# Optimization experiments

Measured on AMD Instinct MI355X. Metric: run time of the kernel, lower is better.

## Reference

```python
import jax, jax.numpy as jnp
import numpy as np

V, T, C, H, L = 32000, 1024, 768, 12, 6
HS = C // H
B = 4
EPS = 1e-5


def layernorm(x, g, b):
    mu = jnp.mean(x, axis=-1, keepdims=True)
    var = jnp.mean(jnp.square(x - mu), axis=-1, keepdims=True)
    return (x - mu) * jax.lax.rsqrt(var + EPS) * g + b


def setup_inputs() -> dict:
    key = jax.random.key(0)
    ks = iter(jax.random.split(key, 24))
    s = lambda *sh: jax.random.normal(next(ks), sh, dtype=jnp.float32) * 0.02
    inp = {
        "tokens": jax.random.randint(next(ks), (B, T), 0, V, dtype=jnp.int64),
        "tok_emb": s(V, C),
        "pos_emb": s(T, C),
        "ln1_g": jnp.ones((L, C), jnp.float32), "ln1_b": jnp.zeros((L, C), jnp.float32),
        "wq": s(L, C, C), "wk": s(L, C, C), "wv": s(L, C, C),
        "wo": s(L, C, C), "bo": jnp.zeros((L, C), jnp.float32),
        "ln2_g": jnp.ones((L, C), jnp.float32), "ln2_b": jnp.zeros((L, C), jnp.float32),
        "w1": s(L, C, 4 * C), "b1": jnp.zeros((L, 4 * C), jnp.float32),
        "w2": s(L, 4 * C, C), "b2": jnp.zeros((L, C), jnp.float32),
        "lnf_g": jnp.ones((C,), jnp.float32), "lnf_b": jnp.zeros((C,), jnp.float32),
        "lm_w": s(C, V), "lm_b": jnp.zeros((V,), jnp.float32),
    }
    return inp


def reference(tokens, tok_emb, pos_emb, ln1_g, ln1_b, wq, wk, wv, wo, bo,
              ln2_g, ln2_b, w1, b1, w2, b2, lnf_g, lnf_b, lm_w, lm_b):
    x = tok_emb[tokens] + pos_emb[:T]  # [B,T,C]
    causal = jnp.tril(jnp.ones((T, T), bool))
    scale = HS ** -0.5
    for l in range(L):
        h = layernorm(x, ln1_g[l], ln1_b[l])
        q = (h @ wq[l]).reshape(B, T, H, HS)
        k = (h @ wk[l]).reshape(B, T, H, HS)
        v = (h @ wv[l]).reshape(B, T, H, HS)
        att = jnp.einsum("bthd,bshd->bhts", q, k) * scale
        att = jnp.where(causal, att, -jnp.inf)
        wei = jax.nn.softmax(att, axis=-1)
        o = jnp.einsum("bhts,bshd->bthd", wei, v).reshape(B, T, C)
        x = o @ wo[l] + bo[l] + x
        h2 = layernorm(x, ln2_g[l], ln2_b[l])
        x = jax.nn.relu(h2 @ w1[l] + b1[l]) @ w2[l] + b2[l] + x
    x = layernorm(x, lnf_g, lnf_b)
    logits = x @ lm_w + lm_b  # [B,T,V]
    return logits
```

## Files before the change

### kernel.cpp

```cpp
#include <hip/hip_runtime.h>

static constexpr int kV = 32000, kT = 1024, kC = 768, kH = 12, kL = 6, kB = 4;
static constexpr int kF = 3072;
static constexpr int kM = kB * kT;
static constexpr float kNEG = -30000.f;

typedef __attribute__((ext_vector_type(8))) __bf16 bf16x8;
typedef __attribute__((ext_vector_type(4))) float  f32x4;

#define DEV __device__ __forceinline__

DEV void gload16(const void* g, void* l) {
  __builtin_amdgcn_global_load_lds((__attribute__((address_space(1))) void*)(g),
                                   (__attribute__((address_space(3))) void*)(l), 16, 0, 0);
}

__global__ __launch_bounds__(192) void embed_k(const int* __restrict__ tokens,
                                               const float* __restrict__ tok_emb,
                                               const float* __restrict__ pos_emb,
                                               float* __restrict__ x) {
  int row = blockIdx.x, tid = threadIdx.x;
  int tok = tokens[row];
  int t   = row & (kT - 1);
  const float4* te = (const float4*)(tok_emb + (size_t)tok * kC);
  const float4* pe = (const float4*)(pos_emb + (size_t)t * kC);
  float4 a = te[tid], p = pe[tid];
  float4 r; r.x = a.x + p.x; r.y = a.y + p.y; r.z = a.z + p.z; r.w = a.w + p.w;
  ((float4*)(x + (size_t)row * kC))[tid] = r;
}

__global__ __launch_bounds__(192) void ln_k(const float* __restrict__ x,
                                            const float* __restrict__ g,
                                            const float* __restrict__ b,
                                            __bf16* __restrict__ out) {
  int row = blockIdx.x, tid = threadIdx.x;
  float4 v = ((const float4*)(x + (size_t)row * kC))[tid];
  float s = v.x + v.y + v.z + v.w;
#pragma unroll
  for (int m = 1; m < 64; m <<= 1) s += __shfl_xor(s, m, 64);
  __shared__ float red1[3], red2[3];
  int wid = tid >> 6;
  if ((tid & 63) == 0) red1[wid] = s;
  __syncthreads();
  float mu = (red1[0] + red1[1] + red1[2]) * (1.f / kC);
  float d0 = v.x - mu, d1 = v.y - mu, d2 = v.z - mu, d3 = v.w - mu;
  float q = d0 * d0 + d1 * d1 + d2 * d2 + d3 * d3;
#pragma unroll
  for (int m = 1; m < 64; m <<= 1) q += __shfl_xor(q, m, 64);
  if ((tid & 63) == 0) red2[wid] = q;
  __syncthreads();
  float var = (red2[0] + red2[1] + red2[2]) * (1.f / kC);
  float rs = rsqrtf(var + 1e-5f);
  float4 gv = ((const float4*)g)[tid];
  float4 bv = ((const float4*)b)[tid];
  float o0 = d0 * rs * gv.x + bv.x;
  float o1 = d1 * rs * gv.y + bv.y;
  float o2 = d2 * rs * gv.z + bv.z;
  float o3 = d3 * rs * gv.w + bv.w;
  ushort4 pk;
  unsigned short* pp = (unsigned short*)&pk;
  __bf16 t0 = (__bf16)o0; pp[0] = *(unsigned short*)&t0;
  __bf16 t1 = (__bf16)o1; pp[1] = *(unsigned short*)&t1;
  __bf16 t2 = (__bf16)o2; pp[2] = *(unsigned short*)&t2;
  __bf16 t3 = (__bf16)o3; pp[3] = *(unsigned short*)&t3;
  ((ushort4*)(out + (size_t)row * kC))[tid] = pk;
}

__global__ __launch_bounds__(256) void convT_k(const float* __restrict__ in,
                                               __bf16* __restrict__ out,
                                               int R, int Cc, size_t in_ls, size_t out_ls) {
  __shared__ float tile[32][33];
  const float* inp  = in  + (size_t)blockIdx.z * in_ls;
  __bf16*      outp = out + (size_t)blockIdx.z * out_ls;
  int r0 = blockIdx.y * 32, c0 = blockIdx.x * 32;
  int tx = threadIdx.x & 31, ty = threadIdx.x >> 5;
#pragma unroll
  for (int i = 0; i < 32; i += 8)
    tile[ty + i][tx] = inp[(size_t)(r0 + ty + i) * Cc + c0 + tx];
  __syncthreads();
  int wx = threadIdx.x & 15, wy = threadIdx.x >> 4;
#pragma unroll
  for (int i = 0; i < 32; i += 16) {
    int oc = wy + i;
    __bf16 a = (__bf16)tile[wx * 2][oc];
    __bf16 c = (__bf16)tile[wx * 2 + 1][oc];
    ushort2 pk;
    unsigned short* pp = (unsigned short*)&pk;
    pp[0] = *(unsigned short*)&a;
    pp[1] = *(unsigned short*)&c;
    *(ushort2*)(&outp[(size_t)(c0 + oc) * R + r0 + wx * 2]) = pk;
  }
}

DEV void tile_decode(int gx, int gy, int& mt, int& nt) {
  int nwg  = gx * gy;
  int wgid = blockIdx.y * gx + blockIdx.x;
  int q8 = nwg >> 3;
  int xcd = wgid & 7, loc = wgid >> 3;
  int sid = xcd * q8 + loc;
  int band = gx << 3;
  int c = sid / band, rem = sid % band;
  nt = rem >> 3;
  mt = (c << 3) + (rem & 7);
}

__global__ __launch_bounds__(512, 1) void gemmHD_k(const __bf16* __restrict__ A,
                                                   const __bf16* __restrict__ Bt,
                                                   const float* __restrict__ bias,
                                                   float* __restrict__ Cout,
                                                   int M, int N, int K) {
  __shared__ char lds[131072];
  int tid = threadIdx.x, lane = tid & 63, wid = tid >> 6;
  int wm = wid >> 2, wn = wid & 3;
  int mt, ntile;
  tile_decode(gridDim.x, gridDim.y, mt, ntile);
  int m0 = mt * 256, n0 = ntile * 256;
  int fr = lane & 15, fg = lane >> 4;
  f32x4 acc[8][4] = {};
  const size_t ldab = (size_t)K * 2;
  int nt = K >> 6;

  auto STAGE = [&](char* base, int t) {
    int k0 = t << 6;
#pragma unroll
    for (int it = 0; it < 4; ++it) {
      int oo  = tid * 16 + it * 8192;
      int row = oo >> 7;
      int cb  = (oo & 127) ^ ((row & 7) << 4);
      gload16((const char*)A + (size_t)(m0 + row) * ldab + (size_t)k0 * 2 + cb,
              base + it * 8192 + wid * 1024);
    }
#pragma unroll
    for (int it = 0; it < 4; ++it) {
      int oo  = tid * 16 + it * 8192;
      int row = oo >> 7;
      int cb  = (oo & 127) ^ ((row & 7) << 4);
      gload16((const char*)Bt + (size_t)(n0 + row) * ldab + (size_t)k0 * 2 + cb,
              base + 32768 + it * 8192 + wid * 1024);
    }
  };

  STAGE(lds, 0);
  asm volatile("s_waitcnt vmcnt(0)" ::: "memory");
  __builtin_amdgcn_sched_barrier(0);
  __builtin_amdgcn_s_barrier();

  for (int t = 0; t < nt; ++t) {
    char* base = lds + (t & 1) * 65536;
    const char* Ab = base;
    const char* Bb = base + 32768;
    if (t + 1 < nt) STAGE(lds + ((t + 1) & 1) * 65536, t + 1);

    __builtin_amdgcn_s_setprio(1);
    bf16x8 bfr[4];
#pragma unroll
    for (int p = 0; p < 4; ++p) {
      const int ks = p >> 1, mh = p & 1;
      const int cc = ks * 64 + fg * 16;
      if (mh == 0) {
#pragma unroll
        for (int n = 0; n < 4; ++n) {
          int row = wn * 64 + n * 16 + fr;
          bfr[n] = *(const bf16x8*)(Bb + row * 128 + (cc ^ ((row & 7) << 4)));
        }
      }
      bf16x8 af[4];
#pragma unroll
      for (int i = 0; i < 4; ++i) {
        int row = wm * 128 + mh * 64 + i * 16 + fr;
        af[i] = *(const bf16x8*)(Ab + row * 128 + (cc ^ ((row & 7) << 4)));
      }
#pragma unroll
      for (int i = 0; i < 4; ++i)
#pragma unroll
        for (int n = 0; n < 4; ++n)
          acc[mh * 4 + i][n] = __builtin_amdgcn_mfma_f32_16x16x32_bf16(
              af[i], bfr[n], acc[mh * 4 + i][n], 0, 0, 0);
    }
    __builtin_amdgcn_s_setprio(0);

    __builtin_amdgcn_s_barrier();
    if (t + 1 < nt)
      asm volatile("s_waitcnt vmcnt(0)" ::: "memory");
    __builtin_amdgcn_sched_barrier(0);
    __builtin_amdgcn_s_barrier();
  }

#pragma unroll
  for (int mi = 0; mi < 8; ++mi) {
#pragma unroll
    for (int n = 0; n < 4; ++n) {
      int cg  = n0 + wn * 64 + n * 16 + fr;
      int rgb = m0 + wm * 128 + mi * 16 + fg * 4;
      float bv = bias[cg];
#pragma unroll
      for (int r = 0; r < 4; ++r)
        Cout[(size_t)(rgb + r) * N + cg] = acc[mi][n][r] + bv;
    }
  }
}

template <int EPI>
__global__ __launch_bounds__(256) void gemm128_k(const __bf16* __restrict__ A,
                                                 const __bf16* __restrict__ Bt,
                                                 const float* __restrict__ bias,
                                                 const float* res,
                                                 void* Cout,
                                                 int M, int N, int K) {
  __shared__ char lds[65536];
  int tid = threadIdx.x, lane = tid & 63, wid = tid >> 6;
  int wr = wid >> 1, wc = wid & 1;
  int mt, ntile;
  tile_decode(gridDim.x, gridDim.y, mt, ntile);
  int m0 = mt * 128, n0 = ntile * 128;
  int fr = lane & 15, fg = lane >> 4;
  f32x4 acc[4][4] = {};
  const size_t ldab = (size_t)K * 2;

  auto STAGE = [&](int buf, int t) {
    int k0 = t << 6;
    char* base = lds + buf * 32768;
#pragma unroll
    for (int it = 0; it < 4; ++it) {
      int oo  = tid * 16 + it * 4096;
      int row = oo >> 7;
      int cb  = (oo & 127) ^ ((row & 7) << 4);
      gload16((const char*)A  + (size_t)(m0 + row) * ldab + (size_t)k0 * 2 + cb,
              base + it * 4096 + wid * 1024);
      gload16((const char*)Bt + (size_t)(n0 + row) * ldab + (size_t)k0 * 2 + cb,
              base + 16384 + it * 4096 + wid * 1024);
    }
  };
  auto COMPUTE = [&](int buf) {
    char* base = lds + buf * 32768;
#pragma unroll
    for (int kk = 0; kk < 2; ++kk) {
      int cb = (kk * 64 + (fg << 4)) ^ ((lane & 7) << 4);
      bf16x8 af[4], bfr[4];
#pragma unroll
      for (int i = 0; i < 4; ++i) {
        af[i]  = *(const bf16x8*)(base         + (wr * 64 + i * 16 + fr) * 128 + cb);
        bfr[i] = *(const bf16x8*)(base + 16384 + (wc * 64 + i * 16 + fr) * 128 + cb);
      }
#pragma unroll
      for (int i = 0; i < 4; ++i)
#pragma unroll
        for (int j = 0; j < 4; ++j)
          acc[i][j] = __builtin_amdgcn_mfma_f32_16x16x32_bf16(af[i], bfr[j], acc[i][j], 0, 0, 0);
    }
  };

  int nt = K >> 6;
  STAGE(0, 0);
  STAGE(1, 1);
  asm volatile("s_waitcnt vmcnt(8)" ::: "memory");
  __builtin_amdgcn_sched_barrier(0);
  __builtin_amdgcn_s_barrier();
  int cur = 0;
  for (int t = 0; t < nt; ++t) {
    __builtin_amdgcn_s_setprio(1);
    COMPUTE(cur);
    __builtin_amdgcn_s_setprio(0);
    if (t + 1 < nt) {
      __builtin_amdgcn_s_barrier();
      if (t + 2 < nt) {
        STAGE(cur, t + 2);
        asm volatile("s_waitcnt vmcnt(8)" ::: "memory");
      } else {
        asm volatile("s_waitcnt vmcnt(0)" ::: "memory");
      }
      __builtin_amdgcn_sched_barrier(0);
      __builtin_amdgcn_s_barrier();
      cur ^= 1;
    }
  }

#pragma unroll
  for (int i = 0; i < 4; ++i) {
#pragma unroll
    for (int j = 0; j < 4; ++j) {
      int cg  = n0 + wc * 64 + j * 16 + fr;
      int rgb = m0 + wr * 64 + i * 16 + fg * 4;
      if constexpr (EPI == 4) {
        if (n0 < 1536) {
#pragma unroll
          for (int r = 0; r < 4; ++r)
            ((__bf16*)Cout)[(size_t)(rgb + r) * 1536 + cg] = (__bf16)acc[i][j][r];
        } else {
          int d = cg - 1536;
          ushort4 pk;
          unsigned short* pp = (unsigned short*)&pk;
#pragma unroll
          for (int r = 0; r < 4; ++r) {
            __bf16 bv = (__bf16)acc[i][j][r];
            pp[r] = *(unsigned short*)&bv;
          }
          __bf16* vT = (__bf16*)const_cast<float*>(res);
          *(ushort4*)(vT + (size_t)d * kM + rgb) = pk;
        }
      } else if constexpr (EPI == 1) {
        float bv = bias[cg];
#pragma unroll
        for (int r = 0; r < 4; ++r) {
          float v = acc[i][j][r] + bv;
          ((__bf16*)Cout)[(size_t)(rgb + r) * N + cg] = (__bf16)fmaxf(v, 0.f);
        }
      } else {
        float bv = bias[cg];
#pragma unroll
        for (int r = 0; r < 4; ++r) {
          float v = acc[i][j][r] + bv;
          size_t idx = (size_t)(rgb + r) * N + cg;
          ((float*)Cout)[idx] = v + res[idx];
        }
      }
    }
  }
}

__global__ __launch_bounds__(256) void attn_k(const __bf16* __restrict__ qk,
                                              const __bf16* __restrict__ vT,
                                              __bf16* __restrict__ optr) {
  __shared__ char lds[40960];
  int tid = threadIdx.x, lane = tid & 63, wid = tid >> 6;
  int hh = blockIdx.y, bb = blockIdx.z;
  int zy = bb * 12 + hh;
  int qt = (blockIdx.x + (zy >> 4) * 5 + (zy & 15)) & 15;
  size_t rowbase = (size_t)bb * kT;
  int qr = qt * 64 + wid * 16;
  char* Psw = lds + 32768 + wid * 2048;

  bf16x8 qf[2];
  {
    const __bf16* p = qk + (rowbase + qr + (lane & 15)) * (2 * kC) + hh * 64 + ((lane >> 4) * 8);
    qf[0] = *(const bf16x8*)p;
    qf[1] = *(const bf16x8*)(p + 32);
  }
  f32x4 oacc[4] = {};
  float mrun[4] = {kNEG, kNEG, kNEG, kNEG};
  float lrun[4] = {0.f, 0.f, 0.f, 0.f};

  bf16x8 kr[2], vr[2];
  auto LOADT = [&](int st) {
    int s0 = st * 64;
#pragma unroll
    for (int it = 0; it < 2; ++it) {
      int oo  = tid * 16 + it * 4096;
      int row = oo >> 7;
      int cb  = (oo & 127) ^ ((row & 7) << 4);
      kr[it] = *(const bf16x8*)((const char*)qk +
                 ((rowbase + s0 + row) * (2 * kC) + kC + hh * 64) * 2 + cb);
      vr[it] = *(const bf16x8*)((const char*)vT +
                 ((size_t)(hh * 64 + row) * kM + rowbase + s0) * 2 + cb);
    }
  };
  auto WRITET = [&](int buf) {
    char* b = lds + buf * 16384;
#pragma unroll
    for (int it = 0; it < 2; ++it) {
      int oo = tid * 16 + it * 4096;
      *(bf16x8*)(b + oo)        = kr[it];
      *(bf16x8*)(b + 8192 + oo) = vr[it];
    }
  };

  LOADT(0);
  WRITET(0);
  if (qt >= 1) LOADT(1);

  for (int st = 0; st <= qt; ++st) {
    int cur = st & 1;
    char* kb = lds + cur * 16384;
    char* vb = kb + 8192;
    __syncthreads();
    if (st + 1 <= qt) {
      WRITET(cur ^ 1);
      if (st + 2 <= qt) LOADT(st + 2);
    }

    int s0 = st * 64;
    f32x4 sacc[4] = {};
#pragma unroll
    for (int kk = 0; kk < 2; ++kk) {
      int cb = (kk * 64 + ((lane >> 4) << 4)) ^ ((lane & 7) << 4);
#pragma unroll
      for (int j = 0; j < 4; ++j) {
        bf16x8 kf = *(const bf16x8*)(kb + (j * 16 + (lane & 15)) * 128 + cb);
        sacc[j] = __builtin_amdgcn_mfma_f32_16x16x32_bf16(qf[kk], kf, sacc[j], 0, 0, 0);
      }
    }

    float pv[4][4], vm[4] = {kNEG, kNEG, kNEG, kNEG};
#pragma unroll
    for (int j = 0; j < 4; ++j) {
      int scol = s0 + j * 16 + (lane & 15);
#pragma unroll
      for (int r = 0; r < 4; ++r) {
        int qrow = qr + (lane >> 4) * 4 + r;
        float sv = sacc[j][r] * 0.125f;
        if (scol > qrow) sv = kNEG;
        pv[j][r] = sv;
        vm[r] = fmaxf(vm[r], sv);
      }
    }
#pragma unroll
    for (int r = 0; r < 4; ++r) {
      float v = vm[r];
      v = fmaxf(v, __shfl_xor(v, 1, 64)); v = fmaxf(v, __shfl_xor(v, 2, 64));
      v = fmaxf(v, __shfl_xor(v, 4, 64)); v = fmaxf(v, __shfl_xor(v, 8, 64));
      float mnew = fmaxf(mrun[r], v);
      float sc = __expf(mrun[r] - mnew);
      mrun[r] = mnew;
      lrun[r] *= sc;
      oacc[0][r] *= sc; oacc[1][r] *= sc; oacc[2][r] *= sc; oacc[3][r] *= sc;
      float rsum = 0.f;
#pragma unroll
      for (int j = 0; j < 4; ++j) {
        float p = __expf(pv[j][r] - mnew);
        pv[j][r] = p;
        rsum += p;
      }
      rsum += __shfl_xor(rsum, 1, 64); rsum += __shfl_xor(rsum, 2, 64);
      rsum += __shfl_xor(rsum, 4, 64); rsum += __shfl_xor(rsum, 8, 64);
      lrun[r] += rsum;
    }

#pragma unroll
    for (int j = 0; j < 4; ++j)
#pragma unroll
      for (int r = 0; r < 4; ++r) {
        int rloc = (lane >> 4) * 4 + r;
        int cbyt = (2 * (j * 16 + (lane & 15))) ^ ((rloc & 7) << 4);
        *(__bf16*)(Psw + rloc * 128 + cbyt) = (__bf16)pv[j][r];
      }

#pragma unroll
    for (int kk = 0; kk < 2; ++kk) {
      int cb = (kk * 64 + ((lane >> 4) << 4)) ^ ((lane & 7) << 4);
      bf16x8 pf = *(const bf16x8*)(Psw + (lane & 15) * 128 + cb);
#pragma unroll
      for (int j = 0; j < 4; ++j) {
        bf16x8 vf = *(const bf16x8*)(vb + (j * 16 + (lane & 15)) * 128 + cb);
        oacc[j] = __builtin_amdgcn_mfma_f32_16x16x32_bf16(pf, vf, oacc[j], 0, 0, 0);
      }
    }
  }

#pragma unroll
  for (int r = 0; r < 4; ++r) {
    float inv = lrun[r] > 0.f ? 1.f / lrun[r] : 0.f;
#pragma unroll
    for (int j = 0; j < 4; ++j) {
      int cg = hh * 64 + j * 16 + (lane & 15);
      int rg = qr + (lane >> 4) * 4 + r;
      optr[(rowbase + rg) * kC + cg] = (__bf16)(oacc[j][r] * inv);
    }
  }
}

extern "C" void kernel_launch(void* const* d_in, const int* in_sizes, int n_in,
                              void* d_out, int out_size, void* d_ws, size_t ws_size,
                              hipStream_t stream) {
  (void)in_sizes; (void)n_in; (void)out_size; (void)ws_size;
  const int*   tokens  = (const int*)  d_in[0];
  const float* tok_emb = (const float*)d_in[1];
  const float* pos_emb = (const float*)d_in[2];
  const float* ln1_g   = (const float*)d_in[3];
  const float* ln1_b   = (const float*)d_in[4];
  const float* wq      = (const float*)d_in[5];
  const float* wk      = (const float*)d_in[6];
  const float* wv      = (const float*)d_in[7];
  const float* wo      = (const float*)d_in[8];
  const float* bo      = (const float*)d_in[9];
  const float* ln2_g   = (const float*)d_in[10];
  const float* ln2_b   = (const float*)d_in[11];
  const float* w1      = (const float*)d_in[12];
  const float* b1      = (const float*)d_in[13];
  const float* w2      = (const float*)d_in[14];
  const float* b2      = (const float*)d_in[15];
  const float* lnf_g   = (const float*)d_in[16];
  const float* lnf_b   = (const float*)d_in[17];
  const float* lm_w    = (const float*)d_in[18];
  const float* lm_b    = (const float*)d_in[19];
  float* out = (float*)d_out;

  char* ws = (char*)d_ws;
  size_t off = 0;
  auto alloc = [&](size_t bytes) -> char* {
    char* p = ws + off; off += (bytes + 255) & ~(size_t)255; return p;
  };
  float*  x    = (float*) alloc((size_t)kM * kC * 4);
  __bf16* h    = (__bf16*)alloc((size_t)kM * kC * 2);
  __bf16* qkvT = (__bf16*)alloc((size_t)kL * 3 * kC * kC * 2);
  __bf16* woT  = (__bf16*)alloc((size_t)kL * kC * kC * 2);
  __bf16* w1T  = (__bf16*)alloc((size_t)kL * kC * kF * 2);
  __bf16* w2T  = (__bf16*)alloc((size_t)kL * kC * kF * 2);
  __bf16* qkb  = (__bf16*)alloc((size_t)kM * 2 * kC * 2);
  __bf16* vTb  = (__bf16*)alloc((size_t)kC * kM * 2);
  __bf16* ob   = (__bf16*)alloc((size_t)kM * kC * 2);
  __bf16* ffb  = (__bf16*)alloc((size_t)kM * kF * 2);
  __bf16* lmwT = qkb;

  dim3 blk(256), blk512(512);
  convT_k<<<dim3(kC/32, kC/32, kL), blk, 0, stream>>>(wq, qkvT,           kC, kC, (size_t)kC*kC, (size_t)3*kC*kC);
  convT_k<<<dim3(kC/32, kC/32, kL), blk, 0, stream>>>(wk, qkvT + kC*kC,   kC, kC, (size_t)kC*kC, (size_t)3*kC*kC);
  convT_k<<<dim3(kC/32, kC/32, kL), blk, 0, stream>>>(wv, qkvT + 2*kC*kC, kC, kC, (size_t)kC*kC, (size_t)3*kC*kC);
  convT_k<<<dim3(kC/32, kC/32, kL), blk, 0, stream>>>(wo, woT,            kC, kC, (size_t)kC*kC, (size_t)kC*kC);
  convT_k<<<dim3(kF/32, kC/32, kL), blk, 0, stream>>>(w1, w1T,            kC, kF, (size_t)kC*kF, (size_t)kC*kF);
  convT_k<<<dim3(kC/32, kF/32, kL), blk, 0, stream>>>(w2, w2T,            kF, kC, (size_t)kC*kF, (size_t)kC*kF);

  embed_k<<<kM, 192, 0, stream>>>(tokens, tok_emb, pos_emb, x);

  for (int l = 0; l < kL; ++l) {
    ln_k<<<kM, 192, 0, stream>>>(x, ln1_g + l*kC, ln1_b + l*kC, h);
    gemm128_k<4><<<dim3(3*kC/128, kM/128), blk, 0, stream>>>(
        h, qkvT + (size_t)l*3*kC*kC, nullptr, (const float*)vTb, qkb, kM, 3*kC, kC);
    attn_k<<<dim3(kT/64, kH, kB), blk, 0, stream>>>(qkb, vTb, ob);
    gemm128_k<2><<<dim3(kC/128, kM/128), blk, 0, stream>>>(ob, woT + (size_t)l*kC*kC, bo + l*kC, x, x, kM, kC, kC);
    ln_k<<<kM, 192, 0, stream>>>(x, ln2_g + l*kC, ln2_b + l*kC, h);
    gemm128_k<1><<<dim3(kF/128, kM/128), blk, 0, stream>>>(h, w1T + (size_t)l*kC*kF, b1 + l*kF, nullptr, ffb, kM, kF, kC);
    gemm128_k<2><<<dim3(kC/128, kM/128), blk, 0, stream>>>(ffb, w2T + (size_t)l*kC*kF, b2 + l*kC, x, x, kM, kC, kF);
  }
  convT_k<<<dim3(kV/32, kC/32, 1), blk, 0, stream>>>(lm_w, lmwT, kC, kV, 0, 0);
  ln_k<<<kM, 192, 0, stream>>>(x, lnf_g, lnf_b, h);
  gemmHD_k<<<dim3(kV/256, kM/256), blk512, 0, stream>>>(h, lmwT, lm_b, out, kM, kV, kC);
}
```

Baseline: 1.418 ms.

## Replace 256x256 LM-head GEMM with 128-tile GEMM and merge QKV weight transposes

```diff
diff --git a/kernel.cpp b/kernel.cpp
--- a/kernel.cpp
+++ b/kernel.cpp
@@ -92,6 +92,34 @@
   }
 }
 
+__global__ __launch_bounds__(256) void convT3_k(const float* __restrict__ wq,
+                                                const float* __restrict__ wk,
+                                                const float* __restrict__ wv,
+                                                __bf16* __restrict__ qkvT) {
+  __shared__ float tile[32][33];
+  int z = blockIdx.z, layer = z / 3, which = z % 3;
+  const float* inp = (which == 0 ? wq : which == 1 ? wk : wv) + (size_t)layer * kC * kC;
+  __bf16* outp = qkvT + (size_t)layer * 3 * kC * kC + (size_t)which * kC * kC;
+  int r0 = blockIdx.y * 32, c0 = blockIdx.x * 32;
+  int tx = threadIdx.x & 31, ty = threadIdx.x >> 5;
+#pragma unroll
+  for (int i = 0; i < 32; i += 8)
+    tile[ty + i][tx] = inp[(size_t)(r0 + ty + i) * kC + c0 + tx];
+  __syncthreads();
+  int wx = threadIdx.x & 15, wy = threadIdx.x >> 4;
+#pragma unroll
+  for (int i = 0; i < 32; i += 16) {
+    int oc = wy + i;
+    __bf16 a = (__bf16)tile[wx * 2][oc];
+    __bf16 c = (__bf16)tile[wx * 2 + 1][oc];
+    ushort2 pk;
+    unsigned short* pp = (unsigned short*)&pk;
+    pp[0] = *(unsigned short*)&a;
+    pp[1] = *(unsigned short*)&c;
+    *(ushort2*)(&outp[(size_t)(c0 + oc) * kC + r0 + wx * 2]) = pk;
+  }
+}
+
 DEV void tile_decode(int gx, int gy, int& mt, int& nt) {
   int nwg  = gx * gy;
   int wgid = blockIdx.y * gx + blockIdx.x;
@@ -102,102 +130,6 @@
   int c = sid / band, rem = sid % band;
   nt = rem >> 3;
   mt = (c << 3) + (rem & 7);
-}
-
-__global__ __launch_bounds__(512, 1) void gemmHD_k(const __bf16* __restrict__ A,
-                                                   const __bf16* __restrict__ Bt,
-                                                   const float* __restrict__ bias,
-                                                   float* __restrict__ Cout,
-                                                   int M, int N, int K) {
-  __shared__ char lds[131072];
-  int tid = threadIdx.x, lane = tid & 63, wid = tid >> 6;
-  int wm = wid >> 2, wn = wid & 3;
-  int mt, ntile;
-  tile_decode(gridDim.x, gridDim.y, mt, ntile);
-  int m0 = mt * 256, n0 = ntile * 256;
-  int fr = lane & 15, fg = lane >> 4;
-  f32x4 acc[8][4] = {};
-  const size_t ldab = (size_t)K * 2;
-  int nt = K >> 6;
-
-  auto STAGE = [&](char* base, int t) {
-    int k0 = t << 6;
-#pragma unroll
-    for (int it = 0; it < 4; ++it) {
-      int oo  = tid * 16 + it * 8192;
-      int row = oo >> 7;
-      int cb  = (oo & 127) ^ ((row & 7) << 4);
-      gload16((const char*)A + (size_t)(m0 + row) * ldab + (size_t)k0 * 2 + cb,
-              base + it * 8192 + wid * 1024);
-    }
-#pragma unroll
-    for (int it = 0; it < 4; ++it) {
-      int oo  = tid * 16 + it * 8192;
-      int row = oo >> 7;
-      int cb  = (oo & 127) ^ ((row & 7) << 4);
-      gload16((const char*)Bt + (size_t)(n0 + row) * ldab + (size_t)k0 * 2 + cb,
-              base + 32768 + it * 8192 + wid * 1024);
-    }
-  };
-
-  STAGE(lds, 0);
-  asm volatile("s_waitcnt vmcnt(0)" ::: "memory");
-  __builtin_amdgcn_sched_barrier(0);
-  __builtin_amdgcn_s_barrier();
-
-  for (int t = 0; t < nt; ++t) {
-    char* base = lds + (t & 1) * 65536;
-    const char* Ab = base;
-    const char* Bb = base + 32768;
-    if (t + 1 < nt) STAGE(lds + ((t + 1) & 1) * 65536, t + 1);
-
-    __builtin_amdgcn_s_setprio(1);
-    bf16x8 bfr[4];
-#pragma unroll
-    for (int p = 0; p < 4; ++p) {
-      const int ks = p >> 1, mh = p & 1;
-      const int cc = ks * 64 + fg * 16;
-      if (mh == 0) {
-#pragma unroll
-        for (int n = 0; n < 4; ++n) {
-          int row = wn * 64 + n * 16 + fr;
-          bfr[n] = *(const bf16x8*)(Bb + row * 128 + (cc ^ ((row & 7) << 4)));
-        }
-      }
-      bf16x8 af[4];
-#pragma unroll
-      for (int i = 0; i < 4; ++i) {
-        int row = wm * 128 + mh * 64 + i * 16 + fr;
-        af[i] = *(const bf16x8*)(Ab + row * 128 + (cc ^ ((row & 7) << 4)));
-      }
-#pragma unroll
-      for (int i = 0; i < 4; ++i)
-#pragma unroll
-        for (int n = 0; n < 4; ++n)
-          acc[mh * 4 + i][n] = __builtin_amdgcn_mfma_f32_16x16x32_bf16(
-              af[i], bfr[n], acc[mh * 4 + i][n], 0, 0, 0);
-    }
-    __builtin_amdgcn_s_setprio(0);
-
-    __builtin_amdgcn_s_barrier();
-    if (t + 1 < nt)
-      asm volatile("s_waitcnt vmcnt(0)" ::: "memory");
-    __builtin_amdgcn_sched_barrier(0);
-    __builtin_amdgcn_s_barrier();
-  }
-
-#pragma unroll
-  for (int mi = 0; mi < 8; ++mi) {
-#pragma unroll
-    for (int n = 0; n < 4; ++n) {
-      int cg  = n0 + wn * 64 + n * 16 + fr;
-      int rgb = m0 + wm * 128 + mi * 16 + fg * 4;
-      float bv = bias[cg];
-#pragma unroll
-      for (int r = 0; r < 4; ++r)
-        Cout[(size_t)(rgb + r) * N + cg] = acc[mi][n][r] + bv;
-    }
-  }
 }
 
 template <int EPI>
@@ -305,6 +237,11 @@
           float v = acc[i][j][r] + bv;
           ((__bf16*)Cout)[(size_t)(rgb + r) * N + cg] = (__bf16)fmaxf(v, 0.f);
         }
+      } else if constexpr (EPI == 3) {
+        float bv = bias[cg];
+#pragma unroll
+        for (int r = 0; r < 4; ++r)
+          ((float*)Cout)[(size_t)(rgb + r) * N + cg] = acc[i][j][r] + bv;
       } else {
         float bv = bias[cg];
 #pragma unroll
@@ -501,13 +438,11 @@
   __bf16* ffb  = (__bf16*)alloc((size_t)kM * kF * 2);
   __bf16* lmwT = qkb;
 
-  dim3 blk(256), blk512(512);
-  convT_k<<<dim3(kC/32, kC/32, kL), blk, 0, stream>>>(wq, qkvT,           kC, kC, (size_t)kC*kC, (size_t)3*kC*kC);
-  convT_k<<<dim3(kC/32, kC/32, kL), blk, 0, stream>>>(wk, qkvT + kC*kC,   kC, kC, (size_t)kC*kC, (size_t)3*kC*kC);
-  convT_k<<<dim3(kC/32, kC/32, kL), blk, 0, stream>>>(wv, qkvT + 2*kC*kC, kC, kC, (size_t)kC*kC, (size_t)3*kC*kC);
-  convT_k<<<dim3(kC/32, kC/32, kL), blk, 0, stream>>>(wo, woT,            kC, kC, (size_t)kC*kC, (size_t)kC*kC);
-  convT_k<<<dim3(kF/32, kC/32, kL), blk, 0, stream>>>(w1, w1T,            kC, kF, (size_t)kC*kF, (size_t)kC*kF);
-  convT_k<<<dim3(kC/32, kF/32, kL), blk, 0, stream>>>(w2, w2T,            kF, kC, (size_t)kC*kF, (size_t)kC*kF);
+  dim3 blk(256);
+  convT3_k<<<dim3(kC/32, kC/32, 3*kL), blk, 0, stream>>>(wq, wk, wv, qkvT);
+  convT_k<<<dim3(kC/32, kC/32, kL), blk, 0, stream>>>(wo, woT, kC, kC, (size_t)kC*kC, (size_t)kC*kC);
+  convT_k<<<dim3(kF/32, kC/32, kL), blk, 0, stream>>>(w1, w1T, kC, kF, (size_t)kC*kF, (size_t)kC*kF);
+  convT_k<<<dim3(kC/32, kF/32, kL), blk, 0, stream>>>(w2, w2T, kF, kC, (size_t)kC*kF, (size_t)kC*kF);
 
   embed_k<<<kM, 192, 0, stream>>>(tokens, tok_emb, pos_emb, x);
 
@@ -523,5 +458,5 @@
   }
   convT_k<<<dim3(kV/32, kC/32, 1), blk, 0, stream>>>(lm_w, lmwT, kC, kV, 0, 0);
   ln_k<<<kM, 192, 0, stream>>>(x, lnf_g, lnf_b, h);
-  gemmHD_k<<<dim3(kV/256, kM/256), blk512, 0, stream>>>(h, lmwT, lm_b, out, kM, kV, kC);
-}
+  gemm128_k<3><<<dim3(kV/128, kM/128), blk, 0, stream>>>(h, lmwT, lm_b, nullptr, out, kM, kV, kC);
+}
```

Result: no change. 1.438 ms (+1.4%).

## Use 128x64-tile GEMM for N=768 residual projections and fuse QKV transposes

Applied to the files above, without the earlier changes.

```diff
diff --git a/kernel.cpp b/kernel.cpp
--- a/kernel.cpp
+++ b/kernel.cpp
@@ -92,6 +92,34 @@
   }
 }
 
+__global__ __launch_bounds__(256) void convT3_k(const float* __restrict__ wq,
+                                                const float* __restrict__ wk,
+                                                const float* __restrict__ wv,
+                                                __bf16* __restrict__ qkvT) {
+  __shared__ float tile[32][33];
+  int z = blockIdx.z, layer = z / 3, which = z % 3;
+  const float* inp = (which == 0 ? wq : which == 1 ? wk : wv) + (size_t)layer * kC * kC;
+  __bf16* outp = qkvT + (size_t)layer * 3 * kC * kC + (size_t)which * kC * kC;
+  int r0 = blockIdx.y * 32, c0 = blockIdx.x * 32;
+  int tx = threadIdx.x & 31, ty = threadIdx.x >> 5;
+#pragma unroll
+  for (int i = 0; i < 32; i += 8)
+    tile[ty + i][tx] = inp[(size_t)(r0 + ty + i) * kC + c0 + tx];
+  __syncthreads();
+  int wx = threadIdx.x & 15, wy = threadIdx.x >> 4;
+#pragma unroll
+  for (int i = 0; i < 32; i += 16) {
+    int oc = wy + i;
+    __bf16 a = (__bf16)tile[wx * 2][oc];
+    __bf16 c = (__bf16)tile[wx * 2 + 1][oc];
+    ushort2 pk;
+    unsigned short* pp = (unsigned short*)&pk;
+    pp[0] = *(unsigned short*)&a;
+    pp[1] = *(unsigned short*)&c;
+    *(ushort2*)(&outp[(size_t)(c0 + oc) * kC + r0 + wx * 2]) = pk;
+  }
+}
+
 DEV void tile_decode(int gx, int gy, int& mt, int& nt) {
   int nwg  = gx * gy;
   int wgid = blockIdx.y * gx + blockIdx.x;
@@ -313,6 +341,104 @@
           size_t idx = (size_t)(rgb + r) * N + cg;
           ((float*)Cout)[idx] = v + res[idx];
         }
+      }
+    }
+  }
+}
+
+__global__ __launch_bounds__(256) void gemm64_k(const __bf16* __restrict__ A,
+                                                const __bf16* __restrict__ Bt,
+                                                const float* __restrict__ bias,
+                                                const float* res,
+                                                float* __restrict__ Cout,
+                                                int M, int N, int K) {
+  __shared__ char lds[49152];
+  int tid = threadIdx.x, lane = tid & 63, wid = tid >> 6;
+  int wr = wid >> 1, wc = wid & 1;
+  int mt, ntile;
+  tile_decode(gridDim.x, gridDim.y, mt, ntile);
+  int m0 = mt * 128, n0 = ntile * 64;
+  int fr = lane & 15, fg = lane >> 4;
+  f32x4 acc[4][2] = {};
+  const size_t ldab = (size_t)K * 2;
+
+  auto STAGE = [&](int buf, int t) {
+    int k0 = t << 6;
+    char* base = lds + buf * 24576;
+#pragma unroll
+    for (int it = 0; it < 4; ++it) {
+      int oo  = tid * 16 + it * 4096;
+      int row = oo >> 7;
+      int cb  = (oo & 127) ^ ((row & 7) << 4);
+      gload16((const char*)A + (size_t)(m0 + row) * ldab + (size_t)k0 * 2 + cb,
+              base + it * 4096 + wid * 1024);
+    }
+#pragma unroll
+    for (int it = 0; it < 2; ++it) {
+      int oo  = tid * 16 + it * 4096;
+      int row = oo >> 7;
+      int cb  = (oo & 127) ^ ((row & 7) << 4);
+      gload16((const char*)Bt + (size_t)(n0 + row) * ldab + (size_t)k0 * 2 + cb,
+              base + 16384 + it * 4096 + wid * 1024);
+    }
+  };
+  auto COMPUTE = [&](int buf) {
+    char* base = lds + buf * 24576;
+#pragma unroll
+    for (int kk = 0; kk < 2; ++kk) {
+      int cb = (kk * 64 + (fg << 4)) ^ ((lane & 7) << 4);
+      bf16x8 af[4], bfr[2];
+#pragma unroll
+      for (int i = 0; i < 4; ++i)
+        af[i] = *(const bf16x8*)(base + (wr * 64 + i * 16 + fr) * 128 + cb);
+#pragma unroll
+      for (int j = 0; j < 2; ++j)
+        bfr[j] = *(const bf16x8*)(base + 16384 + (wc * 32 + j * 16 + fr) * 128 + cb);
+#pragma unroll
+      for (int i = 0; i < 4; ++i)
+#pragma unroll
+        for (int j = 0; j < 2; ++j)
+          acc[i][j] = __builtin_amdgcn_mfma_f32_16x16x32_bf16(af[i], bfr[j], acc[i][j], 0, 0, 0);
+    }
+  };
+
+  int nt = K >> 6;
+  STAGE(0, 0);
+  STAGE(1, 1);
+  asm volatile("s_waitcnt vmcnt(6)" ::: "memory");
+  __builtin_amdgcn_sched_barrier(0);
+  __builtin_amdgcn_s_barrier();
+  int cur = 0;
+  for (int t = 0; t < nt; ++t) {
+    __builtin_amdgcn_s_setprio(1);
+    COMPUTE(cur);
+    __builtin_amdgcn_s_setprio(0);
+    if (t + 1 < nt) {
+      __builtin_amdgcn_s_barrier();
+      if (t + 2 < nt) {
+        STAGE(cur, t + 2);
+        asm volatile("s_waitcnt vmcnt(6)" ::: "memory");
+      } else {
+        asm volatile("s_waitcnt vmcnt(0)" ::: "memory");
+      }
+      __builtin_amdgcn_sched_barrier(0);
+      __builtin_amdgcn_s_barrier();
+      cur ^= 1;
+    }
+  }
+
+#pragma unroll
+  for (int i = 0; i < 4; ++i) {
+#pragma unroll
+    for (int j = 0; j < 2; ++j) {
+      int cg  = n0 + wc * 32 + j * 16 + fr;
+      int rgb = m0 + wr * 64 + i * 16 + fg * 4;
+      float bv = bias[cg];
+#pragma unroll
+      for (int r = 0; r < 4; ++r) {
+        float v = acc[i][j][r] + bv;
+        size_t idx = (size_t)(rgb + r) * N + cg;
+        Cout[idx] = v + res[idx];
       }
     }
   }
@@ -502,12 +628,10 @@
   __bf16* lmwT = qkb;
 
   dim3 blk(256), blk512(512);
-  convT_k<<<dim3(kC/32, kC/32, kL), blk, 0, stream>>>(wq, qkvT,           kC, kC, (size_t)kC*kC, (size_t)3*kC*kC);
-  convT_k<<<dim3(kC/32, kC/32, kL), blk, 0, stream>>>(wk, qkvT + kC*kC,   kC, kC, (size_t)kC*kC, (size_t)3*kC*kC);
-  convT_k<<<dim3(kC/32, kC/32, kL), blk, 0, stream>>>(wv, qkvT + 2*kC*kC, kC, kC, (size_t)kC*kC, (size_t)3*kC*kC);
-  convT_k<<<dim3(kC/32, kC/32, kL), blk, 0, stream>>>(wo, woT,            kC, kC, (size_t)kC*kC, (size_t)kC*kC);
-  convT_k<<<dim3(kF/32, kC/32, kL), blk, 0, stream>>>(w1, w1T,            kC, kF, (size_t)kC*kF, (size_t)kC*kF);
-  convT_k<<<dim3(kC/32, kF/32, kL), blk, 0, stream>>>(w2, w2T,            kF, kC, (size_t)kC*kF, (size_t)kC*kF);
+  convT3_k<<<dim3(kC/32, kC/32, 3*kL), blk, 0, stream>>>(wq, wk, wv, qkvT);
+  convT_k<<<dim3(kC/32, kC/32, kL), blk, 0, stream>>>(wo, woT, kC, kC, (size_t)kC*kC, (size_t)kC*kC);
+  convT_k<<<dim3(kF/32, kC/32, kL), blk, 0, stream>>>(w1, w1T, kC, kF, (size_t)kC*kF, (size_t)kC*kF);
+  convT_k<<<dim3(kC/32, kF/32, kL), blk, 0, stream>>>(w2, w2T, kF, kC, (size_t)kC*kF, (size_t)kC*kF);
 
   embed_k<<<kM, 192, 0, stream>>>(tokens, tok_emb, pos_emb, x);
 
@@ -516,10 +640,10 @@
     gemm128_k<4><<<dim3(3*kC/128, kM/128), blk, 0, stream>>>(
         h, qkvT + (size_t)l*3*kC*kC, nullptr, (const float*)vTb, qkb, kM, 3*kC, kC);
     attn_k<<<dim3(kT/64, kH, kB), blk, 0, stream>>>(qkb, vTb, ob);
-    gemm128_k<2><<<dim3(kC/128, kM/128), blk, 0, stream>>>(ob, woT + (size_t)l*kC*kC, bo + l*kC, x, x, kM, kC, kC);
+    gemm64_k<<<dim3(kC/64, kM/128), blk, 0, stream>>>(ob, woT + (size_t)l*kC*kC, bo + l*kC, x, x, kM, kC, kC);
     ln_k<<<kM, 192, 0, stream>>>(x, ln2_g + l*kC, ln2_b + l*kC, h);
     gemm128_k<1><<<dim3(kF/128, kM/128), blk, 0, stream>>>(h, w1T + (size_t)l*kC*kF, b1 + l*kF, nullptr, ffb, kM, kF, kC);
-    gemm128_k<2><<<dim3(kC/128, kM/128), blk, 0, stream>>>(ffb, w2T + (size_t)l*kC*kF, b2 + l*kC, x, x, kM, kC, kF);
+    gemm64_k<<<dim3(kC/64, kM/128), blk, 0, stream>>>(ffb, w2T + (size_t)l*kC*kF, b2 + l*kC, x, x, kM, kC, kF);
   }
   convT_k<<<dim3(kV/32, kC/32, 1), blk, 0, stream>>>(lm_w, lmwT, kC, kV, 0, 0);
   ln_k<<<kM, 192, 0, stream>>>(x, lnf_g, lnf_b, h);
```

Result: faster. 1.248 ms (-12.0%).
